# Performance work log

Measured on AMD Instinct MI355X. Metric: run time of the kernel, lower is better.

## Reference

```python
import jax, jax.numpy as jnp
import numpy as np

HIDDEN = 1024
N_EXPERTS = 8
TOP_K = 2
INTER = 1408
N_SHARED = 2
SCALE = 1.0  # routed_scaling_factor


def setup_inputs() -> dict:
    key = jax.random.key(0)
    ks = jax.random.split(key, 9)
    s_h = 1.0 / np.sqrt(HIDDEN)
    s_i = 1.0 / np.sqrt(INTER)
    x = jax.random.normal(ks[0], (2, 2048, HIDDEN), dtype=jnp.float32)
    gate_w = jax.random.uniform(ks[1], (N_EXPERTS, HIDDEN), jnp.float32, -s_h, s_h)  # kaiming_uniform-ish
    # routed experts: SwiGLU (gate, up, down), stacked over experts
    wg = jax.random.uniform(ks[2], (N_EXPERTS, HIDDEN, INTER), jnp.float32, -s_h, s_h)
    wu = jax.random.uniform(ks[3], (N_EXPERTS, HIDDEN, INTER), jnp.float32, -s_h, s_h)
    wd = jax.random.uniform(ks[4], (N_EXPERTS, INTER, HIDDEN), jnp.float32, -s_i, s_i)
    # shared experts: one SwiGLU with intermediate = INTER * N_SHARED
    si = INTER * N_SHARED
    s_si = 1.0 / np.sqrt(si)
    swg = jax.random.uniform(ks[5], (HIDDEN, si), jnp.float32, -s_h, s_h)
    swu = jax.random.uniform(ks[6], (HIDDEN, si), jnp.float32, -s_h, s_h)
    swd = jax.random.uniform(ks[7], (si, HIDDEN), jnp.float32, -s_si, s_si)
    return {"x": x, "gate_w": gate_w, "wg": wg, "wu": wu, "wd": wd,
            "swg": swg, "swu": swu, "swd": swd}


def reference(x, gate_w, wg, wu, wd, swg, swu, swd):
    B, S, H = x.shape
    xf = x.reshape(-1, H)                              # [T, H]
    T = xf.shape[0]
    # --- MoEGate (fp32) ---
    logits = xf.astype(jnp.float32) @ gate_w.astype(jnp.float32).T   # [T, E]
    scores = jax.nn.softmax(logits, axis=-1)
    topw, topi = jax.lax.top_k(scores, TOP_K)          # [T, K]
    denom = topw.sum(axis=-1, keepdims=True) + 1e-20   # norm_topk_prob (top_k > 1)
    topw = topw / denom * SCALE
    # dense combine weights [T, E]: zero except at top-k expert slots
    wdense = jnp.zeros((T, N_EXPERTS), jnp.float32).at[
        jnp.arange(T)[:, None], topi].set(topw)
    # --- routed experts (SwiGLU), computed densely per expert and combined ---
    hg = jnp.einsum('th,ehi->eti', xf, wg)             # [E, T, I]
    hu = jnp.einsum('th,ehi->eti', xf, wu)             # [E, T, I]
    eo = jnp.einsum('eti,eih->eth', jax.nn.silu(hg) * hu, wd)   # [E, T, H]
    y = jnp.einsum('te,eth->th', wdense, eo)           # weighted scatter-combine
    # --- shared experts ---
    shared = (jax.nn.silu(xf @ swg) * (xf @ swu)) @ swd
    return (y + shared).reshape(B, S, H)
```

## Files before the change

kernel.cpp:

```cpp
#include <hip/hip_runtime.h>
#include <hip/hip_bf16.h>
#include <math.h>

#define HIDDEN 1024
#define NEXP 8
#define TOPK 2
#define INTER 1408
#define SINTER 2816
#define NTOK 4096
#define NROWS (NTOK * TOPK)
#define NPANEL 10
#define TROWS 16384
#define MAXT 136

typedef unsigned short ushort_t;
typedef __attribute__((ext_vector_type(8))) short short8;
typedef __attribute__((ext_vector_type(4))) float f32x4;

__device__ __forceinline__ ushort_t f2bf(float f) {
    unsigned int b = __float_as_uint(f);
    unsigned int r = (b + 0x7FFFu + ((b >> 16) & 1u)) >> 16;
    return (ushort_t)r;
}
__device__ __forceinline__ float silu_f(float g) {
    return g * (1.0f / (1.0f + __expf(-g)));
}
__device__ __forceinline__ int imin(int a, int b) { return a < b ? a : b; }

#define GLDS16(gp, lp) __builtin_amdgcn_global_load_lds(                     \
    (const __attribute__((address_space(1))) void*)(gp),                     \
    (__attribute__((address_space(3))) void*)(lp), 16, 0, 0)

__global__ void conv_x(const float* __restrict__ src, ushort_t* __restrict__ dst) {
    int i = (blockIdx.x * 256 + threadIdx.x) * 4;
    float4 v = *reinterpret_cast<const float4*>(&src[i]);
    union { ushort_t h[4]; unsigned long long ll; } p;
    p.h[0] = f2bf(v.x); p.h[1] = f2bf(v.y); p.h[2] = f2bf(v.z); p.h[3] = f2bf(v.w);
    *reinterpret_cast<unsigned long long*>(&dst[i]) = p.ll;
}

__global__ void tconv(const float* __restrict__ src, ushort_t* __restrict__ dst,
                      int R, int C, long sstride, long dstride) {
    src += (size_t)blockIdx.z * sstride;
    dst += (size_t)blockIdx.z * dstride;
    __shared__ float tile[32][33];
    int ct = blockIdx.x * 32, rt = blockIdx.y * 32;
    int tx = threadIdx.x, ty = threadIdx.y;
#pragma unroll
    for (int i = 0; i < 4; i++)
        tile[ty + 8 * i][tx] = src[(size_t)(rt + ty + 8 * i) * C + ct + tx];
    __syncthreads();
#pragma unroll
    for (int i = 0; i < 4; i++)
        dst[(size_t)(ct + ty + 8 * i) * R + rt + tx] = f2bf(tile[tx][ty + 8 * i]);
}

__global__ void gate_kernel(const float* __restrict__ x, const float* __restrict__ gw,
                            int* __restrict__ top_i, float* __restrict__ top_w) {
    int t = blockIdx.x;
    int lane = threadIdx.x;
    const float* xr = x + (size_t)t * HIDDEN;
    float acc[NEXP];
#pragma unroll
    for (int e = 0; e < NEXP; e++) acc[e] = 0.f;
    for (int j = 0; j < HIDDEN / 64; j++) {
        float xv = xr[lane + 64 * j];
#pragma unroll
        for (int e = 0; e < NEXP; e++)
            acc[e] = fmaf(xv, gw[e * HIDDEN + lane + 64 * j], acc[e]);
    }
#pragma unroll
    for (int e = 0; e < NEXP; e++) {
        float v = acc[e];
        for (int off = 32; off > 0; off >>= 1) v += __shfl_xor(v, off, 64);
        acc[e] = v;
    }
    if (lane == 0) {
        float mx = acc[0];
        for (int e = 1; e < NEXP; e++) mx = fmaxf(mx, acc[e]);
        float s[NEXP];
        float sum = 0.f;
        for (int e = 0; e < NEXP; e++) { s[e] = __expf(acc[e] - mx); sum += s[e]; }
        float inv = 1.0f / sum;
        for (int e = 0; e < NEXP; e++) s[e] *= inv;
        int e0 = 0;
        for (int e = 1; e < NEXP; e++) if (s[e] > s[e0]) e0 = e;
        int e1 = -1;
        for (int e = 0; e < NEXP; e++) {
            if (e == e0) continue;
            if (e1 < 0 || s[e] > s[e1]) e1 = e;
        }
        float w0 = s[e0], w1 = s[e1];
        float denom = w0 + w1 + 1e-20f;
        top_i[t * 2 + 0] = e0;
        top_i[t * 2 + 1] = e1;
        top_w[t * 2 + 0] = w0 / denom;
        top_w[t * 2 + 1] = w1 / denom;
    }
}

__global__ void assign_kernel(const int* __restrict__ top_i, int* __restrict__ cnt,
                              int* __restrict__ rnk) {
    int j = blockIdx.x * blockDim.x + threadIdx.x;
    if (j < NROWS) rnk[j] = atomicAdd(&cnt[top_i[j]], 1);
}

__global__ void scan_kernel(const int* __restrict__ cnt, int* __restrict__ offs2,
                            int* __restrict__ cnt2, int* __restrict__ task_pm) {
    if (threadIdx.x == 0) {
        int o = 0;
        for (int e = 0; e < NEXP; e++) { offs2[e] = o; cnt2[e] = cnt[e]; o += cnt[e]; }
        offs2[8] = NROWS;          cnt2[8] = NTOK;
        offs2[9] = NROWS + NTOK;   cnt2[9] = NTOK;
        offs2[10] = TROWS;
        int t = 0;
        for (int e = 0; e < NPANEL; e++)
            for (int m0 = 0; m0 < cnt2[e]; m0 += 128)
                task_pm[t++] = (e << 16) | (m0 >> 7);
        for (; t < MAXT; t++) task_pm[t] = -1;
    }
}

__global__ void fill_kernel(const int* __restrict__ top_i, const float* __restrict__ top_w,
                            const int* __restrict__ rnk, const int* __restrict__ offs2,
                            int* __restrict__ tok_of_row, float* __restrict__ w_of_row) {
    int j = blockIdx.x * blockDim.x + threadIdx.x;
    if (j < NROWS) {
        int row = offs2[top_i[j]] + rnk[j];
        tok_of_row[row] = j;
        w_of_row[row] = top_w[j];
    }
}

__global__ void fill_shared(int* __restrict__ tok_of_row, float* __restrict__ w_of_row) {
    int j = blockIdx.x * blockDim.x + threadIdx.x;
    int row = NROWS + j;
    tok_of_row[row] = (j & (NTOK - 1)) << 1;
    w_of_row[row] = 1.0f;
}

__global__ __launch_bounds__(256, 2) void gemm_gu(
    const ushort_t* __restrict__ xb, const ushort_t* __restrict__ WgT,
    const ushort_t* __restrict__ WuT, ushort_t* __restrict__ act,
    const int* __restrict__ tok_of_row, const int* __restrict__ offs2,
    const int* __restrict__ cnt2, const int* __restrict__ task_pm) {
    int tk = task_pm[blockIdx.y];
    if (tk < 0) return;
    int e = tk >> 16;
    int m0 = (tk & 0xffff) << 7;
    int bx = blockIdx.x;
    int mcnt = cnt2[e];
    int base = offs2[e];
    int n0 = bx * 128;
    const ushort_t* Bg = WgT + (size_t)e * INTER * HIDDEN;
    const ushort_t* Bu = WuT + (size_t)e * INTER * HIDDEN;

    __shared__ short As[8 * 512];
    __shared__ short Bgs[8 * 512];
    __shared__ short Bus[8 * 512];

    int tid = threadIdx.x;
    int wave = tid >> 6, lane = tid & 63;
    int wr = wave >> 1, wc = wave & 1;
    int lr = lane & 15;
    int kq = (lane >> 4) * 8;

    int r0 = m0 + 32 * wave + lr, r1 = r0 + 16;
    int rr0 = base + imin(r0, mcnt - 1);
    int rr1 = base + imin(r1, mcnt - 1);
    const ushort_t* srcA0 = xb + (size_t)(tok_of_row[rr0] >> 1) * HIDDEN + kq;
    const ushort_t* srcA1 = xb + (size_t)(tok_of_row[rr1] >> 1) * HIDDEN + kq;
    const ushort_t* srcBg0 = Bg + (size_t)(n0 + 32 * wave + lr) * HIDDEN + kq;
    const ushort_t* srcBg1 = srcBg0 + (size_t)16 * HIDDEN;
    const ushort_t* srcBu0 = Bu + (size_t)(n0 + 32 * wave + lr) * HIDDEN + kq;
    const ushort_t* srcBu1 = srcBu0 + (size_t)16 * HIDDEN;

    f32x4 accG[4][4] = {};
    f32x4 accU[4][4] = {};

    for (int k0 = 0; k0 < HIDDEN; k0 += 32) {
        GLDS16(srcA0 + k0, &As[(2 * wave) * 512]);
        GLDS16(srcA1 + k0, &As[(2 * wave + 1) * 512]);
        GLDS16(srcBg0 + k0, &Bgs[(2 * wave) * 512]);
        GLDS16(srcBg1 + k0, &Bgs[(2 * wave + 1) * 512]);
        GLDS16(srcBu0 + k0, &Bus[(2 * wave) * 512]);
        GLDS16(srcBu1 + k0, &Bus[(2 * wave + 1) * 512]);
        __syncthreads();
        short8 a[4], bg[4], bu[4];
#pragma unroll
        for (int mi = 0; mi < 4; mi++)
            a[mi] = *reinterpret_cast<const short8*>(
                &As[(wr * 4 + mi) * 512 + lane * 8]);
#pragma unroll
        for (int ni = 0; ni < 4; ni++) {
            bg[ni] = *reinterpret_cast<const short8*>(
                &Bgs[(wc * 4 + ni) * 512 + lane * 8]);
            bu[ni] = *reinterpret_cast<const short8*>(
                &Bus[(wc * 4 + ni) * 512 + lane * 8]);
        }
#pragma unroll
        for (int mi = 0; mi < 4; mi++)
#pragma unroll
            for (int ni = 0; ni < 4; ni++) {
                accG[mi][ni] = __builtin_amdgcn_mfma_f32_16x16x32_bf16(
                    a[mi], bg[ni], accG[mi][ni], 0, 0, 0);
                accU[mi][ni] = __builtin_amdgcn_mfma_f32_16x16x32_bf16(
                    a[mi], bu[ni], accU[mi][ni], 0, 0, 0);
            }
        __syncthreads();
    }

#pragma unroll
    for (int mi = 0; mi < 4; mi++) {
#pragma unroll
        for (int r = 0; r < 4; r++) {
            int gm = m0 + wr * 64 + mi * 16 + (lane >> 4) * 4 + r;
            if (gm < mcnt) {
#pragma unroll
                for (int ni = 0; ni < 4; ni++) {
                    int col = n0 + wc * 64 + ni * 16 + lr;
                    float g = accG[mi][ni][r], u = accU[mi][ni][r];
                    act[(size_t)(base + gm) * INTER + col] = f2bf(silu_f(g) * u);
                }
            }
        }
    }
}

__global__ __launch_bounds__(256, 2) void gemm_down(
    const ushort_t* __restrict__ act, const ushort_t* __restrict__ WdT,
    float* __restrict__ out, const int* __restrict__ tok_of_row,
    const float* __restrict__ w_of_row, const int* __restrict__ offs2,
    const int* __restrict__ cnt2, const int* __restrict__ task_pm) {
    int tk = task_pm[blockIdx.y];
    if (tk < 0) return;
    int e = tk >> 16;
    int m0 = (tk & 0xffff) << 7;
    int bx = blockIdx.x;
    int mcnt = cnt2[e];
    int base = offs2[e];
    int n0 = bx * 256;
    const ushort_t* Bd = WdT + (size_t)e * HIDDEN * INTER;

    __shared__ short As[8 * 512];
    __shared__ short Bs[16 * 512];

    int tid = threadIdx.x;
    int wave = tid >> 6, lane = tid & 63;
    int wr = wave >> 1, wc = wave & 1;
    int lr = lane & 15;
    int kq = (lane >> 4) * 8;

    const ushort_t* srcA0 = act + (size_t)(base + m0 + 32 * wave + lr) * INTER + kq;
    const ushort_t* srcA1 = srcA0 + (size_t)16 * INTER;
    const ushort_t* srcB0 = Bd + (size_t)(n0 + 64 * wave + lr) * INTER + kq;
    const ushort_t* srcB1 = srcB0 + (size_t)16 * INTER;
    const ushort_t* srcB2 = srcB0 + (size_t)32 * INTER;
    const ushort_t* srcB3 = srcB0 + (size_t)48 * INTER;

    f32x4 acc[4][8] = {};

    for (int k0 = 0; k0 < INTER; k0 += 32) {
        GLDS16(srcA0 + k0, &As[(2 * wave) * 512]);
        GLDS16(srcA1 + k0, &As[(2 * wave + 1) * 512]);
        GLDS16(srcB0 + k0, &Bs[(4 * wave) * 512]);
        GLDS16(srcB1 + k0, &Bs[(4 * wave + 1) * 512]);
        GLDS16(srcB2 + k0, &Bs[(4 * wave + 2) * 512]);
        GLDS16(srcB3 + k0, &Bs[(4 * wave + 3) * 512]);
        __syncthreads();
        short8 a[4], b[8];
#pragma unroll
        for (int mi = 0; mi < 4; mi++)
            a[mi] = *reinterpret_cast<const short8*>(
                &As[(wr * 4 + mi) * 512 + lane * 8]);
#pragma unroll
        for (int ni = 0; ni < 8; ni++)
            b[ni] = *reinterpret_cast<const short8*>(
                &Bs[(wc * 8 + ni) * 512 + lane * 8]);
#pragma unroll
        for (int mi = 0; mi < 4; mi++)
#pragma unroll
            for (int ni = 0; ni < 8; ni++)
                acc[mi][ni] = __builtin_amdgcn_mfma_f32_16x16x32_bf16(
                    a[mi], b[ni], acc[mi][ni], 0, 0, 0);
        __syncthreads();
    }

#pragma unroll
    for (int mi = 0; mi < 4; mi++) {
#pragma unroll
        for (int r = 0; r < 4; r++) {
            int gm = m0 + wr * 64 + mi * 16 + (lane >> 4) * 4 + r;
            if (gm < mcnt) {
                int tok = tok_of_row[base + gm] >> 1;
                float w = w_of_row[base + gm];
#pragma unroll
                for (int ni = 0; ni < 8; ni++) {
                    int col = n0 + wc * 128 + ni * 16 + lr;
                    atomicAdd(&out[(size_t)tok * HIDDEN + col], w * acc[mi][ni][r]);
                }
            }
        }
    }
}

extern "C" void kernel_launch(void* const* d_in, const int* in_sizes, int n_in,
                              void* d_out, int out_size, void* d_ws, size_t ws_size,
                              hipStream_t stream) {
    const float* x   = (const float*)d_in[0];
    const float* gw  = (const float*)d_in[1];
    const float* wg  = (const float*)d_in[2];
    const float* wu  = (const float*)d_in[3];
    const float* wd  = (const float*)d_in[4];
    const float* swg = (const float*)d_in[5];
    const float* swu = (const float*)d_in[6];
    const float* swd = (const float*)d_in[7];
    float* out = (float*)d_out;

    const size_t XB   = (size_t)NTOK * HIDDEN;
    const size_t WPAN = (size_t)NPANEL * INTER * HIDDEN;
    const size_t ACT  = (size_t)TROWS * INTER;
    ushort_t* xb  = (ushort_t*)d_ws;
    ushort_t* wgT = xb + XB;
    ushort_t* wuT = wgT + WPAN;
    ushort_t* wdT = wuT + WPAN;
    ushort_t* act = wdT + WPAN;
    int* ib = (int*)(act + ACT);
    int* top_i      = ib;
    int* rnk        = ib + NROWS;
    int* cnt        = ib + 2 * NROWS;
    int* offs2      = ib + 2 * NROWS + 8;
    int* cnt2       = offs2 + 16;
    int* task_pm    = cnt2 + 16;
    int* tok_of_row = task_pm + MAXT;
    float* top_w    = (float*)(tok_of_row + TROWS);
    float* w_of_row = top_w + NROWS;

    conv_x<<<(NTOK * HIDDEN) / (256 * 4), 256, 0, stream>>>(x, xb);
    dim3 tb(32, 8);
    tconv<<<dim3(INTER / 32, HIDDEN / 32, NEXP), tb, 0, stream>>>(
        wg, wgT, HIDDEN, INTER, (long)HIDDEN * INTER, (long)INTER * HIDDEN);
    tconv<<<dim3(INTER / 32, HIDDEN / 32, NEXP), tb, 0, stream>>>(
        wu, wuT, HIDDEN, INTER, (long)HIDDEN * INTER, (long)INTER * HIDDEN);
    tconv<<<dim3(SINTER / 32, HIDDEN / 32, 1), tb, 0, stream>>>(
        swg, wgT + (size_t)8 * INTER * HIDDEN, HIDDEN, SINTER, 0, 0);
    tconv<<<dim3(SINTER / 32, HIDDEN / 32, 1), tb, 0, stream>>>(
        swu, wuT + (size_t)8 * INTER * HIDDEN, HIDDEN, SINTER, 0, 0);
    tconv<<<dim3(HIDDEN / 32, INTER / 32, NEXP), tb, 0, stream>>>(
        wd, wdT, INTER, HIDDEN, (long)INTER * HIDDEN, (long)HIDDEN * INTER);
    tconv<<<dim3(HIDDEN / 32, INTER / 32, 2), tb, 0, stream>>>(
        swd, wdT + (size_t)8 * HIDDEN * INTER, INTER, HIDDEN,
        (long)INTER * HIDDEN, (long)HIDDEN * INTER);

    gate_kernel<<<NTOK, 64, 0, stream>>>(x, gw, top_i, top_w);
    hipMemsetAsync(cnt, 0, 8 * sizeof(int), stream);
    assign_kernel<<<NROWS / 256, 256, 0, stream>>>(top_i, cnt, rnk);
    scan_kernel<<<1, 1, 0, stream>>>(cnt, offs2, cnt2, task_pm);
    fill_kernel<<<NROWS / 256, 256, 0, stream>>>(top_i, top_w, rnk, offs2,
                                                 tok_of_row, w_of_row);
    fill_shared<<<NROWS / 256, 256, 0, stream>>>(tok_of_row, w_of_row);

    gemm_gu<<<dim3(INTER / 128, MAXT), 256, 0, stream>>>(
        xb, wgT, wuT, act, tok_of_row, offs2, cnt2, task_pm);
    hipMemsetAsync(out, 0, (size_t)out_size * sizeof(float), stream);
    gemm_down<<<dim3(HIDDEN / 256, MAXT), 256, 0, stream>>>(
        act, wdT, out, tok_of_row, w_of_row, offs2, cnt2, task_pm);
}
```

Measured before the change: 444.0 us.

## Replace atomic scatter in down GEMM with bf16 partials and gather combine

The down-projection GEMM no longer does fp32 atomicAdd scatter into a zeroed output. It writes per-row bf16 partial results, and a new combine kernel gathers the two routed rows (weighted) and two shared panels per token with an inverse row map. The output memset is removed. Both GEMMs also switch to a 1D grid with an XCD-aware block remap, so blocks sharing the same task land on the same XCD for L2 reuse. Partials are rounded to bf16, which lowers precision slightly and adds an extra pass over memory.

```diff
diff --git a/kernel.cpp b/kernel.cpp
--- a/kernel.cpp
+++ b/kernel.cpp
@@ -21,6 +21,9 @@
     unsigned int b = __float_as_uint(f);
     unsigned int r = (b + 0x7FFFu + ((b >> 16) & 1u)) >> 16;
     return (ushort_t)r;
+}
+__device__ __forceinline__ float bf2f(ushort_t u) {
+    return __uint_as_float(((unsigned int)u) << 16);
 }
 __device__ __forceinline__ float silu_f(float g) {
     return g * (1.0f / (1.0f + __expf(-g)));
@@ -123,20 +126,20 @@
 
 __global__ void fill_kernel(const int* __restrict__ top_i, const float* __restrict__ top_w,
                             const int* __restrict__ rnk, const int* __restrict__ offs2,
-                            int* __restrict__ tok_of_row, float* __restrict__ w_of_row) {
+                            int* __restrict__ tok_of_row, float* __restrict__ w_of_row,
+                            int* __restrict__ inv_row) {
     int j = blockIdx.x * blockDim.x + threadIdx.x;
     if (j < NROWS) {
         int row = offs2[top_i[j]] + rnk[j];
         tok_of_row[row] = j;
         w_of_row[row] = top_w[j];
-    }
-}
-
-__global__ void fill_shared(int* __restrict__ tok_of_row, float* __restrict__ w_of_row) {
+        inv_row[j] = row;
+    }
+}
+
+__global__ void fill_shared(int* __restrict__ tok_of_row) {
     int j = blockIdx.x * blockDim.x + threadIdx.x;
-    int row = NROWS + j;
-    tok_of_row[row] = (j & (NTOK - 1)) << 1;
-    w_of_row[row] = 1.0f;
+    tok_of_row[NROWS + j] = (j & (NTOK - 1)) << 1;
 }
 
 __global__ __launch_bounds__(256, 2) void gemm_gu(
@@ -144,14 +147,18 @@
     const ushort_t* __restrict__ WuT, ushort_t* __restrict__ act,
     const int* __restrict__ tok_of_row, const int* __restrict__ offs2,
     const int* __restrict__ cnt2, const int* __restrict__ task_pm) {
-    int tk = task_pm[blockIdx.y];
+    int T = gridDim.x;
+    int orig = blockIdx.x;
+    int logical = (orig & 7) * (T >> 3) + (orig >> 3);
+    int task = logical % MAXT;
+    int nidx = logical / MAXT;
+    int tk = task_pm[task];
     if (tk < 0) return;
     int e = tk >> 16;
     int m0 = (tk & 0xffff) << 7;
-    int bx = blockIdx.x;
     int mcnt = cnt2[e];
     int base = offs2[e];
-    int n0 = bx * 128;
+    int n0 = nidx * 128;
     const ushort_t* Bg = WgT + (size_t)e * INTER * HIDDEN;
     const ushort_t* Bu = WuT + (size_t)e * INTER * HIDDEN;
 
@@ -229,17 +236,20 @@
 
 __global__ __launch_bounds__(256, 2) void gemm_down(
     const ushort_t* __restrict__ act, const ushort_t* __restrict__ WdT,
-    float* __restrict__ out, const int* __restrict__ tok_of_row,
-    const float* __restrict__ w_of_row, const int* __restrict__ offs2,
+    ushort_t* __restrict__ part, const int* __restrict__ offs2,
     const int* __restrict__ cnt2, const int* __restrict__ task_pm) {
-    int tk = task_pm[blockIdx.y];
+    int T = gridDim.x;
+    int orig = blockIdx.x;
+    int logical = (orig & 7) * (T >> 3) + (orig >> 3);
+    int task = logical % MAXT;
+    int nidx = logical / MAXT;
+    int tk = task_pm[task];
     if (tk < 0) return;
     int e = tk >> 16;
     int m0 = (tk & 0xffff) << 7;
-    int bx = blockIdx.x;
     int mcnt = cnt2[e];
     int base = offs2[e];
-    int n0 = bx * 256;
+    int n0 = nidx * 256;
     const ushort_t* Bd = WdT + (size_t)e * HIDDEN * INTER;
 
     __shared__ short As[8 * 512];
@@ -292,16 +302,33 @@
         for (int r = 0; r < 4; r++) {
             int gm = m0 + wr * 64 + mi * 16 + (lane >> 4) * 4 + r;
             if (gm < mcnt) {
-                int tok = tok_of_row[base + gm] >> 1;
-                float w = w_of_row[base + gm];
 #pragma unroll
                 for (int ni = 0; ni < 8; ni++) {
                     int col = n0 + wc * 128 + ni * 16 + lr;
-                    atomicAdd(&out[(size_t)tok * HIDDEN + col], w * acc[mi][ni][r]);
+                    part[(size_t)(base + gm) * HIDDEN + col] = f2bf(acc[mi][ni][r]);
                 }
             }
         }
     }
+}
+
+__global__ __launch_bounds__(256) void combine_kernel(
+    const ushort_t* __restrict__ part, const int* __restrict__ inv_row,
+    const float* __restrict__ w_of_row, float* __restrict__ out) {
+    int t = blockIdx.x;
+    int c = threadIdx.x * 4;
+    int r0 = inv_row[2 * t], r1 = inv_row[2 * t + 1];
+    float w0 = w_of_row[r0], w1 = w_of_row[r1];
+    ushort4 a0 = *reinterpret_cast<const ushort4*>(&part[(size_t)r0 * HIDDEN + c]);
+    ushort4 a1 = *reinterpret_cast<const ushort4*>(&part[(size_t)r1 * HIDDEN + c]);
+    ushort4 a2 = *reinterpret_cast<const ushort4*>(&part[((size_t)NROWS + t) * HIDDEN + c]);
+    ushort4 a3 = *reinterpret_cast<const ushort4*>(&part[((size_t)NROWS + NTOK + t) * HIDDEN + c]);
+    float4 o;
+    o.x = w0 * bf2f(a0.x) + w1 * bf2f(a1.x) + bf2f(a2.x) + bf2f(a3.x);
+    o.y = w0 * bf2f(a0.y) + w1 * bf2f(a1.y) + bf2f(a2.y) + bf2f(a3.y);
+    o.z = w0 * bf2f(a0.z) + w1 * bf2f(a1.z) + bf2f(a2.z) + bf2f(a3.z);
+    o.w = w0 * bf2f(a0.w) + w1 * bf2f(a1.w) + bf2f(a2.w) + bf2f(a3.w);
+    *reinterpret_cast<float4*>(&out[(size_t)t * HIDDEN + c]) = o;
 }
 
 extern "C" void kernel_launch(void* const* d_in, const int* in_sizes, int n_in,
@@ -320,12 +347,14 @@
     const size_t XB   = (size_t)NTOK * HIDDEN;
     const size_t WPAN = (size_t)NPANEL * INTER * HIDDEN;
     const size_t ACT  = (size_t)TROWS * INTER;
-    ushort_t* xb  = (ushort_t*)d_ws;
-    ushort_t* wgT = xb + XB;
-    ushort_t* wuT = wgT + WPAN;
-    ushort_t* wdT = wuT + WPAN;
-    ushort_t* act = wdT + WPAN;
-    int* ib = (int*)(act + ACT);
+    const size_t PART = (size_t)TROWS * HIDDEN;
+    ushort_t* xb   = (ushort_t*)d_ws;
+    ushort_t* wgT  = xb + XB;
+    ushort_t* wuT  = wgT + WPAN;
+    ushort_t* wdT  = wuT + WPAN;
+    ushort_t* act  = wdT + WPAN;
+    ushort_t* part = act + ACT;
+    int* ib = (int*)(part + PART);
     int* top_i      = ib;
     int* rnk        = ib + NROWS;
     int* cnt        = ib + 2 * NROWS;
@@ -333,7 +362,8 @@
     int* cnt2       = offs2 + 16;
     int* task_pm    = cnt2 + 16;
     int* tok_of_row = task_pm + MAXT;
-    float* top_w    = (float*)(tok_of_row + TROWS);
+    int* inv_row    = tok_of_row + TROWS;
+    float* top_w    = (float*)(inv_row + NROWS);
     float* w_of_row = top_w + NROWS;
 
     conv_x<<<(NTOK * HIDDEN) / (256 * 4), 256, 0, stream>>>(x, xb);
@@ -357,12 +387,12 @@
     assign_kernel<<<NROWS / 256, 256, 0, stream>>>(top_i, cnt, rnk);
     scan_kernel<<<1, 1, 0, stream>>>(cnt, offs2, cnt2, task_pm);
     fill_kernel<<<NROWS / 256, 256, 0, stream>>>(top_i, top_w, rnk, offs2,
-                                                 tok_of_row, w_of_row);
-    fill_shared<<<NROWS / 256, 256, 0, stream>>>(tok_of_row, w_of_row);
-
-    gemm_gu<<<dim3(INTER / 128, MAXT), 256, 0, stream>>>(
+                                                 tok_of_row, w_of_row, inv_row);
+    fill_shared<<<NROWS / 256, 256, 0, stream>>>(tok_of_row);
+
+    gemm_gu<<<MAXT * (INTER / 128), 256, 0, stream>>>(
         xb, wgT, wuT, act, tok_of_row, offs2, cnt2, task_pm);
-    hipMemsetAsync(out, 0, (size_t)out_size * sizeof(float), stream);
-    gemm_down<<<dim3(HIDDEN / 256, MAXT), 256, 0, stream>>>(
-        act, wdT, out, tok_of_row, w_of_row, offs2, cnt2, task_pm);
-}
+    gemm_down<<<MAXT * (HIDDEN / 256), 256, 0, stream>>>(
+        act, wdT, part, offs2, cnt2, task_pm);
+    combine_kernel<<<NTOK, 256, 0, stream>>>(part, inv_row, w_of_row, out);
+}
```

New measurement: 397.0 us. 1.12x faster.
